# Performance work log

Hardware: AMD Instinct MI355X
Metric: run time of the kernel (lower is better)

The kernel has to match this reference:

```python
import jax, jax.numpy as jnp
import numpy as np

PAD_ID = 0  # tokenizer.pad_token_id (Llama branch => num_padding_at_beginning = 0)


def _first_true(x, default):
    """Index of first True along axis 1 of bool [B,S]; `default` if none."""
    has = x.any(axis=1)
    return jnp.where(has, jnp.argmax(x, axis=1), default)


def setup_inputs() -> dict:
    key = jax.random.key(0)
    k1, k2, k3, k4, k5 = jax.random.split(key, 5)
    B, S, H, V = 16, 4096, 1024, 32000
    return {
        "chosen_ids": jax.random.randint(k1, (B, S), 0, V, dtype=jnp.int32),
        "chosen_mask": jnp.ones((B, S), dtype=jnp.int32),
        "rejected_ids": jax.random.randint(k2, (B, S), 0, V, dtype=jnp.int32),
        "chosen_hidden": jax.random.normal(k3, (B, S, H), dtype=jnp.float32),
        "rejected_hidden": jax.random.normal(k4, (B, S, H), dtype=jnp.float32),
        "v_head_w": jax.random.normal(k5, (H,), dtype=jnp.float32) * (1.0 / np.sqrt(H)),
    }


def reference(chosen_ids, chosen_mask, rejected_ids, chosen_hidden, rejected_hidden, v_head_w):
    B, S = chosen_ids.shape
    seq_len = S  # chosen/rejected share the same padded length

    # v_head: [B,S,H] @ [H] -> [B,S] per-token rewards
    chosen_rewards = jnp.einsum("bsh,h->bs", chosen_hidden, v_head_w)
    rejected_rewards = jnp.einsum("bsh,h->bs", rejected_hidden, v_head_w)

    pos = jnp.arange(S)[None, :]                      # [1,S]
    start_ind = jnp.argmax(chosen_mask != 0, axis=1)  # first nonzero of mask, [B]

    # first PAD at/after start (num_padding_at_beginning == 0), else seq_len
    c_pad = (chosen_ids == PAD_ID) & (pos >= start_ind[:, None])
    c_ind = _first_true(c_pad, seq_len)               # [B]
    r_pad = (rejected_ids == PAD_ID) & (pos >= start_ind[:, None])
    r_ind_div = _first_true(r_pad, seq_len)           # [B]

    has_div = (chosen_ids != rejected_ids).any(axis=1)
    # no-divergence branch: r_ind = min(c_ind, seq_len)
    r_ind = jnp.where(has_div, r_ind_div, jnp.minimum(c_ind, seq_len))
    # final: c_ind = min(c_ind, r_ind); r_ind = min(c_ind, r_ind) -> both collapse
    last = jnp.minimum(c_ind, r_ind) - 1              # score position, [B]

    b = jnp.arange(B)
    chosen_mean_scores = chosen_rewards[b, last]
    rejected_mean_scores = rejected_rewards[b, last]
    loss = jnp.mean(-jax.nn.log_sigmoid(chosen_mean_scores - rejected_mean_scores))
    return loss, chosen_mean_scores, rejected_mean_scores
```

## Files before the change

### kernel.cpp

```cpp
#include <hip/hip_runtime.h>
#include <math.h>
#include <limits.h>

#define BB 16
#define SS 4096
#define HH 1024
#define PAD_ID 0

__global__ __launch_bounds__(256) void find_last_kernel(
    const int* __restrict__ chosen_ids,
    const int* __restrict__ chosen_mask,
    const int* __restrict__ rejected_ids,
    int* __restrict__ last_out,
    float* __restrict__ out)
{
    const int b = blockIdx.x;
    const int t = threadIdx.x;
    const int* cid = chosen_ids   + (size_t)b * SS;
    const int* msk = chosen_mask  + (size_t)b * SS;
    const int* rid = rejected_ids + (size_t)b * SS;

    __shared__ int s1[256];
    __shared__ int s2[256];
    __shared__ int s3[256];
    __shared__ int s_start;

    int mymin = INT_MAX;
    for (int i = t; i < SS; i += 256) {
        if (msk[i] != 0) { mymin = i; break; }
    }
    s1[t] = mymin;
    __syncthreads();
    for (int ofs = 128; ofs > 0; ofs >>= 1) {
        if (t < ofs) s1[t] = min(s1[t], s1[t + ofs]);
        __syncthreads();
    }
    if (t == 0) s_start = (s1[0] == INT_MAX) ? 0 : s1[0];
    __syncthreads();
    const int start = s_start;
    __syncthreads();

    int cmin = INT_MAX, rmin = INT_MAX, diff = 0;
    for (int i = t; i < SS; i += 256) {
        int c = cid[i];
        int r = rid[i];
        diff |= (c != r);
        if (i >= start) {
            if (c == PAD_ID && i < cmin) cmin = i;
            if (r == PAD_ID && i < rmin) rmin = i;
        }
    }
    s1[t] = cmin; s2[t] = rmin; s3[t] = diff;
    __syncthreads();
    for (int ofs = 128; ofs > 0; ofs >>= 1) {
        if (t < ofs) {
            s1[t] = min(s1[t], s1[t + ofs]);
            s2[t] = min(s2[t], s2[t + ofs]);
            s3[t] |= s3[t + ofs];
        }
        __syncthreads();
    }
    if (t == 0) {
        int c_ind = (s1[0] == INT_MAX) ? SS : s1[0];
        int r_div = (s2[0] == INT_MAX) ? SS : s2[0];
        int r_ind = s3[0] ? r_div : c_ind;
        int last  = min(c_ind, r_ind) - 1;
        if (last < 0) last += SS;
        last_out[b] = last;
        if (b == 0) out[0] = 0.0f;
    }
}

__global__ __launch_bounds__(256) void score_kernel(
    const float* __restrict__ chosen_hidden,
    const float* __restrict__ rejected_hidden,
    const float* __restrict__ w,
    const int* __restrict__ last_in,
    float* __restrict__ out)
{
    const int b = blockIdx.x;
    const int t = threadIdx.x;
    const int last = last_in[b];

    const float4* ch = (const float4*)(chosen_hidden   + ((size_t)b * SS + last) * HH);
    const float4* rh = (const float4*)(rejected_hidden + ((size_t)b * SS + last) * HH);
    const float4* wv = (const float4*)w;

    float4 c4 = ch[t];
    float4 r4 = rh[t];
    float4 w4 = wv[t];
    float cs = c4.x * w4.x + c4.y * w4.y + c4.z * w4.z + c4.w * w4.w;
    float rs = r4.x * w4.x + r4.y * w4.y + r4.z * w4.z + r4.w * w4.w;

    __shared__ float sc[256];
    __shared__ float sr[256];
    sc[t] = cs; sr[t] = rs;
    __syncthreads();
    for (int ofs = 128; ofs > 0; ofs >>= 1) {
        if (t < ofs) { sc[t] += sc[t + ofs]; sr[t] += sr[t + ofs]; }
        __syncthreads();
    }
    if (t == 0) {
        float c = sc[0];
        float r = sr[0];
        out[1 + b]      = c;
        out[1 + BB + b] = r;
        float x  = r - c;
        float sp = fmaxf(x, 0.0f) + log1pf(expf(-fabsf(x)));
        atomicAdd(out, sp * (1.0f / BB));
    }
}

extern "C" void kernel_launch(void* const* d_in, const int* in_sizes, int n_in,
                              void* d_out, int out_size, void* d_ws, size_t ws_size,
                              hipStream_t stream) {
    const int*   chosen_ids      = (const int*)d_in[0];
    const int*   chosen_mask     = (const int*)d_in[1];
    const int*   rejected_ids    = (const int*)d_in[2];
    const float* chosen_hidden   = (const float*)d_in[3];
    const float* rejected_hidden = (const float*)d_in[4];
    const float* v_head_w        = (const float*)d_in[5];
    float* out = (float*)d_out;
    int*   last_ws = (int*)d_ws;

    find_last_kernel<<<BB, 256, 0, stream>>>(chosen_ids, chosen_mask, rejected_ids,
                                             last_ws, out);
    score_kernel<<<BB, 256, 0, stream>>>(chosen_hidden, rejected_hidden, v_head_w,
                                         last_ws, out);
}
```

Measured before the change: 412.6 us.

## Fuse index search and scoring into one kernel with vectorized loads and wave shuffles

Merges the pad-index search and the v_head dot product into a single kernel per batch row. Token ids and the mask are now read as int4 in one batch of loads, and the tree reductions in shared memory are replaced with wavefront shuffle reductions. The loss is summed by a small second kernel instead of atomics. The aim is to cut launch overhead, barriers and uncoalesced scalar loads, at the cost of more registers per thread and a tiny extra launch.

```diff
diff --git a/kernel.cpp b/kernel.cpp
--- a/kernel.cpp
+++ b/kernel.cpp
@@ -7,108 +7,122 @@
 #define HH 1024
 #define PAD_ID 0
 
-__global__ __launch_bounds__(256) void find_last_kernel(
-    const int* __restrict__ chosen_ids,
-    const int* __restrict__ chosen_mask,
-    const int* __restrict__ rejected_ids,
-    int* __restrict__ last_out,
-    float* __restrict__ out)
+__global__ __launch_bounds__(256) void fused_kernel(
+    const int*   __restrict__ chosen_ids,
+    const int*   __restrict__ chosen_mask,
+    const int*   __restrict__ rejected_ids,
+    const float* __restrict__ chosen_hidden,
+    const float* __restrict__ rejected_hidden,
+    const float* __restrict__ w,
+    float* __restrict__ out,
+    float* __restrict__ sp_ws)
 {
     const int b = blockIdx.x;
     const int t = threadIdx.x;
-    const int* cid = chosen_ids   + (size_t)b * SS;
-    const int* msk = chosen_mask  + (size_t)b * SS;
-    const int* rid = rejected_ids + (size_t)b * SS;
 
-    __shared__ int s1[256];
-    __shared__ int s2[256];
-    __shared__ int s3[256];
-    __shared__ int s_start;
+    const int4* msk4 = (const int4*)(chosen_mask  + (size_t)b * SS);
+    const int4* cid4 = (const int4*)(chosen_ids   + (size_t)b * SS);
+    const int4* rid4 = (const int4*)(rejected_ids + (size_t)b * SS);
 
-    int mymin = INT_MAX;
-    for (int i = t; i < SS; i += 256) {
-        if (msk[i] != 0) { mymin = i; break; }
+    const float4 w4 = ((const float4*)w)[t];
+
+    int4 m[4], c[4], r[4];
+#pragma unroll
+    for (int k = 0; k < 4; ++k) {
+        m[k] = msk4[k * 256 + t];
+        c[k] = cid4[k * 256 + t];
+        r[k] = rid4[k * 256 + t];
     }
-    s1[t] = mymin;
+
+    int mstart = INT_MAX;
+#pragma unroll
+    for (int k = 0; k < 4; ++k) {
+        const int base = k * 1024 + t * 4;
+        const int v0 = m[k].x, v1 = m[k].y, v2 = m[k].z, v3 = m[k].w;
+        if (v0) mstart = min(mstart, base + 0);
+        if (v1) mstart = min(mstart, base + 1);
+        if (v2) mstart = min(mstart, base + 2);
+        if (v3) mstart = min(mstart, base + 3);
+    }
+    __shared__ int sM[4];
+#pragma unroll
+    for (int ofs = 32; ofs > 0; ofs >>= 1)
+        mstart = min(mstart, __shfl_xor(mstart, ofs, 64));
+    if ((t & 63) == 0) sM[t >> 6] = mstart;
     __syncthreads();
-    for (int ofs = 128; ofs > 0; ofs >>= 1) {
-        if (t < ofs) s1[t] = min(s1[t], s1[t + ofs]);
-        __syncthreads();
-    }
-    if (t == 0) s_start = (s1[0] == INT_MAX) ? 0 : s1[0];
-    __syncthreads();
-    const int start = s_start;
-    __syncthreads();
+    int start = min(min(sM[0], sM[1]), min(sM[2], sM[3]));
+    if (start == INT_MAX) start = 0;
 
     int cmin = INT_MAX, rmin = INT_MAX, diff = 0;
-    for (int i = t; i < SS; i += 256) {
-        int c = cid[i];
-        int r = rid[i];
-        diff |= (c != r);
-        if (i >= start) {
-            if (c == PAD_ID && i < cmin) cmin = i;
-            if (r == PAD_ID && i < rmin) rmin = i;
+#pragma unroll
+    for (int k = 0; k < 4; ++k) {
+        const int base = k * 1024 + t * 4;
+        const int cv[4] = { c[k].x, c[k].y, c[k].z, c[k].w };
+        const int rv[4] = { r[k].x, r[k].y, r[k].z, r[k].w };
+#pragma unroll
+        for (int j = 0; j < 4; ++j) {
+            const int i = base + j;
+            diff |= (cv[j] != rv[j]);
+            if (i >= start) {
+                if (cv[j] == PAD_ID) cmin = min(cmin, i);
+                if (rv[j] == PAD_ID) rmin = min(rmin, i);
+            }
         }
     }
-    s1[t] = cmin; s2[t] = rmin; s3[t] = diff;
+    __shared__ int sA[4], sB[4], sC[4];
+#pragma unroll
+    for (int ofs = 32; ofs > 0; ofs >>= 1) {
+        cmin = min(cmin, __shfl_xor(cmin, ofs, 64));
+        rmin = min(rmin, __shfl_xor(rmin, ofs, 64));
+        diff |= __shfl_xor(diff, ofs, 64);
+    }
+    if ((t & 63) == 0) { const int wv = t >> 6; sA[wv] = cmin; sB[wv] = rmin; sC[wv] = diff; }
     __syncthreads();
-    for (int ofs = 128; ofs > 0; ofs >>= 1) {
-        if (t < ofs) {
-            s1[t] = min(s1[t], s1[t + ofs]);
-            s2[t] = min(s2[t], s2[t + ofs]);
-            s3[t] |= s3[t + ofs];
-        }
-        __syncthreads();
+    cmin = min(min(sA[0], sA[1]), min(sA[2], sA[3]));
+    rmin = min(min(sB[0], sB[1]), min(sB[2], sB[3]));
+    diff = sC[0] | sC[1] | sC[2] | sC[3];
+
+    const int c_ind = (cmin == INT_MAX) ? SS : cmin;
+    const int r_div = (rmin == INT_MAX) ? SS : rmin;
+    const int r_ind = diff ? r_div : c_ind;
+    int last = min(c_ind, r_ind) - 1;
+    if (last < 0) last += SS;
+
+    const float4* ch = (const float4*)(chosen_hidden   + ((size_t)b * SS + last) * HH);
+    const float4* rh = (const float4*)(rejected_hidden + ((size_t)b * SS + last) * HH);
+    const float4 c4 = ch[t];
+    const float4 r4 = rh[t];
+    float cs = c4.x * w4.x + c4.y * w4.y + c4.z * w4.z + c4.w * w4.w;
+    float rs = r4.x * w4.x + r4.y * w4.y + r4.z * w4.z + r4.w * w4.w;
+
+    __shared__ float sF[4], sG[4];
+#pragma unroll
+    for (int ofs = 32; ofs > 0; ofs >>= 1) {
+        cs += __shfl_xor(cs, ofs, 64);
+        rs += __shfl_xor(rs, ofs, 64);
     }
+    if ((t & 63) == 0) { const int wv = t >> 6; sF[wv] = cs; sG[wv] = rs; }
+    __syncthreads();
     if (t == 0) {
-        int c_ind = (s1[0] == INT_MAX) ? SS : s1[0];
-        int r_div = (s2[0] == INT_MAX) ? SS : s2[0];
-        int r_ind = s3[0] ? r_div : c_ind;
-        int last  = min(c_ind, r_ind) - 1;
-        if (last < 0) last += SS;
-        last_out[b] = last;
-        if (b == 0) out[0] = 0.0f;
+        const float cscore = sF[0] + sF[1] + sF[2] + sF[3];
+        const float rscore = sG[0] + sG[1] + sG[2] + sG[3];
+        out[1 + b]      = cscore;
+        out[1 + BB + b] = rscore;
+        const float x  = rscore - cscore;
+        sp_ws[b] = fmaxf(x, 0.0f) + log1pf(expf(-fabsf(x)));
     }
 }
 
-__global__ __launch_bounds__(256) void score_kernel(
-    const float* __restrict__ chosen_hidden,
-    const float* __restrict__ rejected_hidden,
-    const float* __restrict__ w,
-    const int* __restrict__ last_in,
+__global__ __launch_bounds__(64) void loss_kernel(
+    const float* __restrict__ sp_ws,
     float* __restrict__ out)
 {
-    const int b = blockIdx.x;
     const int t = threadIdx.x;
-    const int last = last_in[b];
-
-    const float4* ch = (const float4*)(chosen_hidden   + ((size_t)b * SS + last) * HH);
-    const float4* rh = (const float4*)(rejected_hidden + ((size_t)b * SS + last) * HH);
-    const float4* wv = (const float4*)w;
-
-    float4 c4 = ch[t];
-    float4 r4 = rh[t];
-    float4 w4 = wv[t];
-    float cs = c4.x * w4.x + c4.y * w4.y + c4.z * w4.z + c4.w * w4.w;
-    float rs = r4.x * w4.x + r4.y * w4.y + r4.z * w4.z + r4.w * w4.w;
-
-    __shared__ float sc[256];
-    __shared__ float sr[256];
-    sc[t] = cs; sr[t] = rs;
-    __syncthreads();
-    for (int ofs = 128; ofs > 0; ofs >>= 1) {
-        if (t < ofs) { sc[t] += sc[t + ofs]; sr[t] += sr[t + ofs]; }
-        __syncthreads();
-    }
-    if (t == 0) {
-        float c = sc[0];
-        float r = sr[0];
-        out[1 + b]      = c;
-        out[1 + BB + b] = r;
-        float x  = r - c;
-        float sp = fmaxf(x, 0.0f) + log1pf(expf(-fabsf(x)));
-        atomicAdd(out, sp * (1.0f / BB));
-    }
+    float v = (t < BB) ? sp_ws[t] : 0.0f;
+#pragma unroll
+    for (int ofs = 32; ofs > 0; ofs >>= 1)
+        v += __shfl_xor(v, ofs, 64);
+    if (t == 0) out[0] = v * (1.0f / BB);
 }
 
 extern "C" void kernel_launch(void* const* d_in, const int* in_sizes, int n_in,
@@ -120,11 +134,11 @@
     const float* chosen_hidden   = (const float*)d_in[3];
     const float* rejected_hidden = (const float*)d_in[4];
     const float* v_head_w        = (const float*)d_in[5];
-    float* out = (float*)d_out;
-    int*   last_ws = (int*)d_ws;
+    float* out   = (float*)d_out;
+    float* sp_ws = (float*)d_ws;
 
-    find_last_kernel<<<BB, 256, 0, stream>>>(chosen_ids, chosen_mask, rejected_ids,
-                                             last_ws, out);
-    score_kernel<<<BB, 256, 0, stream>>>(chosen_hidden, rejected_hidden, v_head_w,
-                                         last_ws, out);
+    fused_kernel<<<BB, 256, 0, stream>>>(chosen_ids, chosen_mask, rejected_ids,
+                                         chosen_hidden, rejected_hidden, v_head_w,
+                                         out, sp_ws);
+    loss_kernel<<<1, 64, 0, stream>>>(sp_ws, out);
 }
```

New measurement: 405.7 us. No clear change (-1.7%).
